# Performance work log

Hardware: AMD Instinct MI355X
Metric: run time of the kernel (lower is better)

## Reference

```python
import jax, jax.numpy as jnp
import numpy as np

B, N, C, H = 16, 577, 768, 12
D = C // H
BETA = 1.0
KEEP_RATIO = 0.5


def setup_inputs() -> dict:
    key = jax.random.key(0)
    k0, k1, k2, k3 = jax.random.split(key, 4)
    x = jax.random.normal(k0, (B, N, C), dtype=jnp.float32)
    # UCB visit-count buffer, strictly positive as accumulated counts would be
    ucb_count_score = jax.random.uniform(k1, (H, N), dtype=jnp.float32) * 50.0 + 1.0
    Wqkv = jax.random.normal(k2, (3 * C, C), dtype=jnp.float32) * 0.02
    Wproj = jax.random.normal(k3, (C, C), dtype=jnp.float32) * 0.02
    bproj = jnp.zeros((C,), dtype=jnp.float32)
    counter = 60  # > 50 so pruning path is taken
    return {"x": x, "ucb_count_score": ucb_count_score, "Wqkv": Wqkv,
            "Wproj": Wproj, "bproj": bproj, "counter": counter}


def reference(x, ucb_count_score, Wqkv, Wproj, bproj, counter):
    # UCBAttention.forward with pruning_enabled=True, selection_mode='ucb',
    # ucb_update_enabled=True, exclude_cls=True, dropout=0 (eval).
    Bs, Ns, Cs = x.shape
    scale = D ** -0.5
    k_keep = max(1, int((Ns - 1) * KEEP_RATIO))  # _get_k with keep_ratio

    qkv = (x @ Wqkv.T).reshape(Bs, Ns, 3, H, D).transpose(2, 0, 3, 1, 4)  # [3,B,H,N,D]
    q, k, v = qkv[0], qkv[1], qkv[2]
    attn_scores = jnp.einsum('bhqd,bhkd->bhqk', q, k) * scale
    attn_probs = jax.nn.softmax(attn_scores, axis=-1)  # [B,H,N,N]

    # UCB scores over patches (CLS excluded)
    patch_scores = attn_probs[:, :, :, 1:].mean(axis=2)            # [B,H,N-1]
    expl = BETA * jnp.sqrt(jnp.log(counter + 1.0) / (ucb_count_score[:, 1:] + 1e-6))
    ucb_scores = patch_scores + expl[None, :, :]                   # [B,H,N-1]
    global_ucb = ucb_scores.mean(axis=1)                           # [B,N-1]
    _, topk_rel = jax.lax.top_k(global_ucb, k_keep)                # [B,k]
    kept = topk_rel + 1                                            # token indices

    # keep-vector: CLS (0) always kept; mask[i,j] = kept[i] OR kept[j]
    kv_mask = (jnp.zeros((Bs, Ns), attn_probs.dtype)
               .at[jnp.arange(Bs)[:, None], kept].set(1.0)
               .at[:, 0].set(1.0))                                 # [B,N]
    mask = jnp.maximum(kv_mask[:, None, :, None], kv_mask[:, None, None, :])  # [B,1,N,N]

    pruned = attn_probs * mask
    pruned = pruned / (pruned.sum(axis=-1, keepdims=True) + 1e-8)
    context = jnp.einsum('bhqk,bhkd->bhqd', pruned, v)             # [B,H,N,D]

    out = context.transpose(0, 2, 1, 3).reshape(Bs, Ns, Cs) @ Wproj.T + bproj

    # score_delta: +1/B at each kept token column, broadcast over heads
    delta = jnp.zeros((Ns,), jnp.float32).at[kept.reshape(-1)].add(1.0 / Bs)
    score_delta = jnp.broadcast_to(delta[None, :], ucb_count_score.shape)
    return out, score_delta, kept
```

## Files before the change

### kernel.cpp

```cpp
#include <hip/hip_runtime.h>
#include <cstdio>
#include <cstdint>

#define B_    16
#define N_    577
#define C_    768
#define H_    12
#define D_    64
#define KKEEP 288
#define SCALE 0.125f
#define LOG2E 1.4426950408889634f
#define M_TOT (B_ * N_)
#define NKT   24
#define PLROW ((size_t)N_ * 64)

typedef __bf16 bf16x8_t __attribute__((ext_vector_type(8)));
typedef __bf16 bf16x4_t __attribute__((ext_vector_type(4)));
typedef float  f32x4_t  __attribute__((ext_vector_type(4)));
typedef unsigned int u32x4_t __attribute__((ext_vector_type(4)));
typedef unsigned int u32x2_t __attribute__((ext_vector_type(2)));

__device__ __forceinline__ f32x4_t mfma_bf16(bf16x8_t a, bf16x8_t b, f32x4_t c) {
    return __builtin_amdgcn_mfma_f32_16x16x32_bf16(a, b, c, 0, 0, 0);
}

__device__ __forceinline__ void gload16(const ushort* g, ushort* l) {
    __builtin_amdgcn_global_load_lds(
        (const __attribute__((address_space(1))) void*)g,
        (__attribute__((address_space(3))) void*)l, 16, 0, 0);
}
#define VMCNT(n) asm volatile("s_waitcnt vmcnt(" #n ")" ::: "memory")
#define LGKM0()  asm volatile("s_waitcnt lgkmcnt(0)" ::: "memory")
#define SB() __builtin_amdgcn_sched_barrier(0)

__device__ __forceinline__ int xcd_swz(int bid, int nwg) {
    int q = nwg >> 3, r = nwg & 7;
    int xcd = bid & 7, off = bid >> 3;
    int base = (xcd < r) ? xcd * (q + 1) : r * (q + 1) + (xcd - r) * q;
    return base + off;
}

__device__ __forceinline__ void splitf(float x, unsigned int &hi, unsigned int &lo) {
    unsigned int u = __float_as_uint(x);
    hi = u >> 16;
    float r = x - __uint_as_float(u & 0xffff0000u);
    lo = __float_as_uint(r) >> 16;
}
__device__ __forceinline__ unsigned int bf16rne(float x) {
    unsigned int u = __float_as_uint(x);
    return (u + 0x7fffu + ((u >> 16) & 1u)) >> 16;
}

__device__ __forceinline__ void pack_tile(const float* __restrict__ src,
                                          ushort* __restrict__ dH,
                                          ushort* __restrict__ dL,
                                          int nrows, int tile) {
    int kt = tile % NKT, mt = tile / NKT;
    int w = threadIdx.x;
    int row = w >> 1, h = w & 1;
    int m = mt * 128 + row;
    int sw = (row >> 1) & 3;
    float f[16];
    if (m < nrows) {
        const float* s = src + (size_t)m * C_ + kt * 32;
        int sa = (2 * h) ^ sw, sb = (2 * h + 1) ^ sw;
        *(float4*)&f[0]  = *(const float4*)(s + sa * 8);
        *(float4*)&f[4]  = *(const float4*)(s + sa * 8 + 4);
        *(float4*)&f[8]  = *(const float4*)(s + sb * 8);
        *(float4*)&f[12] = *(const float4*)(s + sb * 8 + 4);
    } else {
#pragma unroll
        for (int i = 0; i < 16; i++) f[i] = 0.f;
    }
    unsigned hi[16], lo[16];
#pragma unroll
    for (int i = 0; i < 16; i++) splitf(f[i], hi[i], lo[i]);
    u32x4_t h0 = {hi[0] | (hi[1] << 16), hi[2] | (hi[3] << 16),
                  hi[4] | (hi[5] << 16), hi[6] | (hi[7] << 16)};
    u32x4_t h1 = {hi[8] | (hi[9] << 16), hi[10] | (hi[11] << 16),
                  hi[12] | (hi[13] << 16), hi[14] | (hi[15] << 16)};
    u32x4_t l0 = {lo[0] | (lo[1] << 16), lo[2] | (lo[3] << 16),
                  lo[4] | (lo[5] << 16), lo[6] | (lo[7] << 16)};
    u32x4_t l1 = {lo[8] | (lo[9] << 16), lo[10] | (lo[11] << 16),
                  lo[12] | (lo[13] << 16), lo[14] | (lo[15] << 16)};
    size_t dbase = (size_t)tile * 4096 + row * 32;
    *(u32x4_t*)&dH[dbase + (2 * h) * 8]     = h0;
    *(u32x4_t*)&dH[dbase + (2 * h + 1) * 8] = h1;
    *(u32x4_t*)&dL[dbase + (2 * h) * 8]     = l0;
    *(u32x4_t*)&dL[dbase + (2 * h + 1) * 8] = l1;
}

__device__ __forceinline__ void pack_tile_rne(const float* __restrict__ src,
                                              ushort* __restrict__ dst,
                                              int nrows, int tile) {
    int kt = tile % NKT, mt = tile / NKT;
    int w = threadIdx.x;
    int row = w >> 1, h = w & 1;
    int m = mt * 128 + row;
    int sw = (row >> 1) & 3;
    float f[16];
    if (m < nrows) {
        const float* s = src + (size_t)m * C_ + kt * 32;
        int sa = (2 * h) ^ sw, sb = (2 * h + 1) ^ sw;
        *(float4*)&f[0]  = *(const float4*)(s + sa * 8);
        *(float4*)&f[4]  = *(const float4*)(s + sa * 8 + 4);
        *(float4*)&f[8]  = *(const float4*)(s + sb * 8);
        *(float4*)&f[12] = *(const float4*)(s + sb * 8 + 4);
    } else {
#pragma unroll
        for (int i = 0; i < 16; i++) f[i] = 0.f;
    }
    unsigned hi[16];
#pragma unroll
    for (int i = 0; i < 16; i++) hi[i] = bf16rne(f[i]);
    u32x4_t h0 = {hi[0] | (hi[1] << 16), hi[2] | (hi[3] << 16),
                  hi[4] | (hi[5] << 16), hi[6] | (hi[7] << 16)};
    u32x4_t h1 = {hi[8] | (hi[9] << 16), hi[10] | (hi[11] << 16),
                  hi[12] | (hi[13] << 16), hi[14] | (hi[15] << 16)};
    size_t dbase = (size_t)tile * 4096 + row * 32;
    *(u32x4_t*)&dst[dbase + (2 * h) * 8]     = h0;
    *(u32x4_t*)&dst[dbase + (2 * h + 1) * 8] = h1;
}

#define NXP 1752
#define NWP 432
#define NPJ 144
#define NZ  37

__global__ __launch_bounds__(256) void pack_all_kernel(const float* __restrict__ x,
                                                       const float* __restrict__ Wqkv,
                                                       const float* __restrict__ Wproj,
                                                       ushort* __restrict__ XplH,
                                                       ushort* __restrict__ XplL,
                                                       ushort* __restrict__ WplH,
                                                       ushort* __restrict__ WplL,
                                                       ushort* __restrict__ Wpjb,
                                                       float* __restrict__ kvmask) {
    int bid = blockIdx.x;
    if (bid < NXP) {
        pack_tile(x, XplH, XplL, M_TOT, bid);
    } else if (bid < NXP + NWP) {
        pack_tile(Wqkv, WplH, WplL, 3 * C_, bid - NXP);
    } else if (bid < NXP + NWP + NPJ) {
        pack_tile_rne(Wproj, Wpjb, C_, bid - NXP - NWP);
    } else {
        int i = (bid - NXP - NWP - NPJ) * 256 + threadIdx.x;
        if (i < B_ * N_) kvmask[i] = 0.f;
    }
}

__device__ __forceinline__ bf16x8_t fragT(const ushort* H, int row, int c, int ls) {
    int phys = ((c << 2) + ls) ^ (row & 7);
    return __builtin_bit_cast(bf16x8_t, *(const u32x4_t*)&H[(row << 6) + (phys << 3)]);
}

__global__ __launch_bounds__(256) void gemm_qkv_mfma(const ushort* __restrict__ XplH,
                                                     const ushort* __restrict__ XplL,
                                                     const ushort* __restrict__ WplH,
                                                     const ushort* __restrict__ WplL,
                                                     ushort* __restrict__ qhp,
                                                     ushort* __restrict__ qlp,
                                                     ushort* __restrict__ khp,
                                                     ushort* __restrict__ klp,
                                                     ushort* __restrict__ vtp) {
    __shared__ ushort SMEM[32768];
    ushort* Ah = SMEM;
    ushort* Al = SMEM + 8192;
    ushort* Bh = SMEM + 16384;
    ushort* Bl = SMEM + 24576;
    const int bid = xcd_swz(blockIdx.x, 18 * 73);
    const int bx = bid % 18, by = bid / 18;
    const int tid = threadIdx.x;
    const int lane = tid & 63, wave = tid >> 6;
    const int wr = wave >> 1, wc = wave & 1;
    const int lr = lane & 15, ls = lane >> 4;
    const int m0 = by * 128;
    const int o0 = wave * 1024, o1 = o0 + 512;
    const int la = lane * 8;
    const size_t abase = (size_t)by * NKT * 4096;
    const size_t bbase = (size_t)bx * NKT * 4096;
    f32x4_t acc[4][4] = {};

    if (bx < 12) {
        auto stage = [&](int buf, int kt) {
            const size_t ta = abase + (size_t)kt * 4096;
            const size_t tb = bbase + (size_t)kt * 4096;
            gload16(XplH + ta + o0 + la, &Ah[buf * 4096 + o0]);
            gload16(XplH + ta + o1 + la, &Ah[buf * 4096 + o1]);
            gload16(XplL + ta + o0 + la, &Al[buf * 4096 + o0]);
            gload16(XplL + ta + o1 + la, &Al[buf * 4096 + o1]);
            gload16(WplH + tb + o0 + la, &Bh[buf * 4096 + o0]);
            gload16(WplH + tb + o1 + la, &Bh[buf * 4096 + o1]);
            gload16(WplL + tb + o0 + la, &Bl[buf * 4096 + o0]);
            gload16(WplL + tb + o1 + la, &Bl[buf * 4096 + o1]);
        };
        stage(0, 0);
#pragma unroll 1
        for (int kt = 0; kt < NKT; ++kt) {
            const int cur = kt & 1;
            if (kt + 1 < NKT) {
                stage(cur ^ 1, kt + 1);
                VMCNT(8);
            } else {
                VMCNT(0);
            }
            SB();
            __builtin_amdgcn_s_barrier();
            SB();
            bf16x8_t fah[4], fal[4], fbh[4], fbl[4];
#pragma unroll
            for (int i = 0; i < 4; i++) {
                int rowA = wr * 64 + i * 16 + lr;
                int pa = ls ^ ((rowA >> 1) & 3);
                fah[i] = __builtin_bit_cast(bf16x8_t, *(const u32x4_t*)&Ah[cur * 4096 + rowA * 32 + pa * 8]);
                fal[i] = __builtin_bit_cast(bf16x8_t, *(const u32x4_t*)&Al[cur * 4096 + rowA * 32 + pa * 8]);
                int rowB = wc * 64 + i * 16 + lr;
                int pb = ls ^ ((rowB >> 1) & 3);
                fbh[i] = __builtin_bit_cast(bf16x8_t, *(const u32x4_t*)&Bh[cur * 4096 + rowB * 32 + pb * 8]);
                fbl[i] = __builtin_bit_cast(bf16x8_t, *(const u32x4_t*)&Bl[cur * 4096 + rowB * 32 + pb * 8]);
            }
#pragma unroll
            for (int i = 0; i < 4; i++)
#pragma unroll
                for (int j = 0; j < 4; j++) {
                    acc[i][j] = mfma_bf16(fah[i], fbh[j], acc[i][j]);
                    acc[i][j] = mfma_bf16(fah[i], fbl[j], acc[i][j]);
                    acc[i][j] = mfma_bf16(fal[i], fbh[j], acc[i][j]);
                }
            if (kt + 1 < NKT) {
                SB();
                __builtin_amdgcn_s_barrier();
            }
        }
        const int n0 = bx * 128;
        const int s = n0 / C_;
        __syncthreads();
        unsigned* T = (unsigned*)SMEM;
        const float sc = (s == 0) ? SCALE * LOG2E : 1.0f;
#pragma unroll
        for (int j = 0; j < 4; j++) {
            int nl = wc * 64 + j * 16 + lr;
#pragma unroll
            for (int i = 0; i < 4; i++) {
#pragma unroll
                for (int r = 0; r < 4; r++) {
                    int ml = wr * 64 + i * 16 + ls * 4 + r;
                    unsigned hi, lo;
                    splitf(acc[i][j][r] * sc, hi, lo);
                    int idx = ml * 128 + ((((nl >> 3) ^ ((ml >> 2) & 7)) << 3) | (nl & 7));
                    T[idx] = hi | (lo << 16);
                }
            }
        }
        __syncthreads();
        ushort* dh = (s == 1) ? khp : qhp;
        ushort* dl = (s == 1) ? klp : qlp;
        const int hh0 = (n0 % C_) / D_;
#pragma unroll
        for (int it = 0; it < 8; ++it) {
            int g = it * 256 + tid;
            int sl = g & 7;
            int m_local = (g >> 3) & 127;
            int hh_half = g >> 10;
            int m = m0 + m_local;
            if (m < M_TOT) {
                int b = m / N_, n = m % N_;
                int dg = sl ^ (n & 7);
                int grp = (hh_half * 8 + dg) ^ ((m_local >> 2) & 7);
                const unsigned* src = &T[m_local * 128 + grp * 8];
                u32x4_t a = *(const u32x4_t*)src;
                u32x4_t bvv = *(const u32x4_t*)(src + 4);
                u32x4_t hiv = {(a[0] & 0xffffu) | (a[1] << 16),
                               (a[2] & 0xffffu) | (a[3] << 16),
                               (bvv[0] & 0xffffu) | (bvv[1] << 16),
                               (bvv[2] & 0xffffu) | (bvv[3] << 16)};
                u32x4_t lov = {(a[0] >> 16) | (a[1] & 0xffff0000u),
                               (a[2] >> 16) | (a[3] & 0xffff0000u),
                               (bvv[0] >> 16) | (bvv[1] & 0xffff0000u),
                               (bvv[2] >> 16) | (bvv[3] & 0xffff0000u)};
                size_t off = (size_t)(b * H_ + hh0 + hh_half) * PLROW + (size_t)n * 64 + sl * 8;
                *(u32x4_t*)&dh[off] = hiv;
                *(u32x4_t*)&dl[off] = lov;
            }
        }
    } else {
        auto stage = [&](int buf, int kt) {
            const size_t ta = abase + (size_t)kt * 4096;
            const size_t tb = bbase + (size_t)kt * 4096;
            gload16(XplH + ta + o0 + la, &Ah[buf * 4096 + o0]);
            gload16(XplH + ta + o1 + la, &Ah[buf * 4096 + o1]);
            gload16(XplL + ta + o0 + la, &Al[buf * 4096 + o0]);
            gload16(XplL + ta + o1 + la, &Al[buf * 4096 + o1]);
            gload16(WplH + tb + o0 + la, &Bh[buf * 4096 + o0]);
            gload16(WplH + tb + o1 + la, &Bh[buf * 4096 + o1]);
        };
        stage(0, 0);
#pragma unroll 1
        for (int kt = 0; kt < NKT; ++kt) {
            const int cur = kt & 1;
            if (kt + 1 < NKT) {
                stage(cur ^ 1, kt + 1);
                VMCNT(6);
            } else {
                VMCNT(0);
            }
            SB();
            __builtin_amdgcn_s_barrier();
            SB();
            bf16x8_t fah[4], fal[4], fbh[4];
#pragma unroll
            for (int i = 0; i < 4; i++) {
                int rowA = wr * 64 + i * 16 + lr;
                int pa = ls ^ ((rowA >> 1) & 3);
                fah[i] = __builtin_bit_cast(bf16x8_t, *(const u32x4_t*)&Ah[cur * 4096 + rowA * 32 + pa * 8]);
                fal[i] = __builtin_bit_cast(bf16x8_t, *(const u32x4_t*)&Al[cur * 4096 + rowA * 32 + pa * 8]);
                int rowB = wc * 64 + i * 16 + lr;
                int pb = ls ^ ((rowB >> 1) & 3);
                fbh[i] = __builtin_bit_cast(bf16x8_t, *(const u32x4_t*)&Bh[cur * 4096 + rowB * 32 + pb * 8]);
            }
#pragma unroll
            for (int i = 0; i < 4; i++)
#pragma unroll
                for (int j = 0; j < 4; j++) {
                    acc[i][j] = mfma_bf16(fah[i], fbh[j], acc[i][j]);
                    acc[i][j] = mfma_bf16(fal[i], fbh[j], acc[i][j]);
                }
            if (kt + 1 < NKT) {
                SB();
                __builtin_amdgcn_s_barrier();
            }
        }
        const int n0v = (bx - 12) * 128;
#pragma unroll
        for (int j = 0; j < 4; j++) {
            int ng = n0v + wc * 64 + j * 16 + lr;
            int hh = ng / D_;
            int d = ng % D_;
#pragma unroll
            for (int i = 0; i < 4; i++) {
                int mg0 = m0 + wr * 64 + i * 16 + ls * 4;
#pragma unroll
                for (int r = 0; r < 4; r++) {
                    int m = mg0 + r;
                    if (m < M_TOT) {
                        int b = m / N_, n = m % N_;
                        int jt = n >> 6, jl = n & 63;
                        size_t off = ((size_t)(b * H_ + hh) * 10 + jt) * 4096 +
                                     (size_t)d * 64 + (((jl >> 3) ^ (d & 7)) << 3) + (jl & 7);
                        vtp[off] = __builtin_bit_cast(unsigned short, (__bf16)acc[i][j][r]);
                    }
                }
            }
        }
    }
}

__global__ __launch_bounds__(512) void attn_rowsum_mfma(const ushort* __restrict__ qh,
                                                        const ushort* __restrict__ ql,
                                                        const ushort* __restrict__ kh,
                                                        const ushort* __restrict__ kl,
                                                        float* __restrict__ w) {
    __shared__ ushort Qh[8192], Ql[8192];
    __shared__ ushort Kh[4096], Kl[4096];
    __shared__ float red[8][64];
    const int bid = xcd_swz(blockIdx.x, 5 * B_ * H_);
    const int bh = bid / 5, q0 = (bid % 5) * 128;
    const int tid = threadIdx.x, lane = tid & 63, wv = tid >> 6;
    const int wg = wv >> 2, wl = wv & 3;
    const int lr = lane & 15, ls = lane >> 4;
    const size_t bho = (size_t)bh * PLROW;
    const ushort* qhp = qh + bho; const ushort* qlp = ql + bho;
    const ushort* khp = kh + bho; const ushort* klp = kl + bho;
    auto qrow = [&](int rr) { return (size_t)min(q0 + wv * 16 + rr * 8 + (lane >> 3), N_ - 1) * 64 + (lane & 7) * 8; };
    gload16(qhp + qrow(0), &Qh[wv * 1024]);
    gload16(qhp + qrow(1), &Qh[wv * 1024 + 512]);
    gload16(qlp + qrow(0), &Ql[wv * 1024]);
    gload16(qlp + qrow(1), &Ql[wv * 1024 + 512]);
    auto krow = [&](int j0) { return (size_t)min(j0 + wv * 8 + (lane >> 3), N_ - 1) * 64 + (lane & 7) * 8; };
    auto stageK = [&](int j0) {
        gload16(khp + krow(j0), &Kh[wv * 512]);
        gload16(klp + krow(j0), &Kl[wv * 512]);
    };
    stageK(0);
    VMCNT(0);
    __syncthreads();
    bf16x8_t fqh[4][2], fql[4][2];
#pragma unroll
    for (int i = 0; i < 4; i++)
#pragma unroll
        for (int c = 0; c < 2; c++) {
            fqh[i][c] = fragT(Qh, wg * 64 + i * 16 + lr, c, ls);
            fql[i][c] = fragT(Ql, wg * 64 + i * 16 + lr, c, ls);
        }
    float rs[4] = {0.f, 0.f, 0.f, 0.f};
#pragma unroll 1
    for (int t = 0; t < 10; ++t) {
        bf16x8_t fkh[2], fkl[2];
#pragma unroll
        for (int c = 0; c < 2; c++) {
            fkh[c] = fragT(Kh, wl * 16 + lr, c, ls);
            fkl[c] = fragT(Kl, wl * 16 + lr, c, ls);
        }
        LGKM0(); SB();
        __builtin_amdgcn_s_barrier();
        SB();
        if (t < 9) stageK((t + 1) * 64);
        int jbase = t * 64 + wl * 16 + ls * 4;
#pragma unroll
        for (int i = 0; i < 4; i++) {
            f32x4_t s = {0.f, 0.f, 0.f, 0.f};
            __builtin_amdgcn_s_setprio(1);
#pragma unroll
            for (int c = 0; c < 2; c++) {
                s = mfma_bf16(fkh[c], fqh[i][c], s);
                s = mfma_bf16(fkh[c], fql[i][c], s);
                s = mfma_bf16(fkl[c], fqh[i][c], s);
            }
            __builtin_amdgcn_s_setprio(0);
#pragma unroll
            for (int r = 0; r < 4; r++)
                rs[i] += (jbase + r < N_) ? __builtin_amdgcn_exp2f(s[r]) : 0.f;
        }
        if (t < 9) {
            VMCNT(0); SB();
            __builtin_amdgcn_s_barrier();
            SB();
        }
    }
#pragma unroll
    for (int i = 0; i < 4; i++) {
        float v2 = rs[i];
        v2 += __shfl_xor(v2, 16);
        v2 += __shfl_xor(v2, 32);
        if (ls == 0) red[wv][i * 16 + lr] = v2;
    }
    __syncthreads();
    if (tid < 128) {
        int grp = tid >> 6, qlc = tid & 63;
        float s = red[grp * 4 + 0][qlc] + red[grp * 4 + 1][qlc] +
                  red[grp * 4 + 2][qlc] + red[grp * 4 + 3][qlc];
        int qn = q0 + tid;
        if (qn < N_) w[(size_t)bh * N_ + qn] = 1.0f / s;
    }
}

__global__ __launch_bounds__(512) void attn_colsum_mfma(const ushort* __restrict__ qh,
                                                        const ushort* __restrict__ ql,
                                                        const ushort* __restrict__ kh,
                                                        const ushort* __restrict__ kl,
                                                        const float* __restrict__ w,
                                                        float* __restrict__ colsum) {
    __shared__ ushort KhS[8192], KlS[8192];
    __shared__ ushort Qh[4096], Ql[4096];
    __shared__ float wsAll[640];
    __shared__ float red[8][64];
    const int bid = xcd_swz(blockIdx.x, 5 * B_ * H_);
    const int bh = bid / 5, j0 = (bid % 5) * 128;
    const int tid = threadIdx.x, lane = tid & 63, wv = tid >> 6;
    const int wg = wv >> 2, wl = wv & 3;
    const int lr = lane & 15, ls = lane >> 4;
    const size_t bho = (size_t)bh * PLROW;
    const ushort* qhp = qh + bho; const ushort* qlp = ql + bho;
    const ushort* khp = kh + bho; const ushort* klp = kl + bho;
    auto krow = [&](int rr) { return (size_t)min(j0 + wv * 16 + rr * 8 + (lane >> 3), N_ - 1) * 64 + (lane & 7) * 8; };
    gload16(khp + krow(0), &KhS[wv * 1024]);
    gload16(khp + krow(1), &KhS[wv * 1024 + 512]);
    gload16(klp + krow(0), &KlS[wv * 1024]);
    gload16(klp + krow(1), &KlS[wv * 1024 + 512]);
    auto qrow2 = [&](int qt) { return (size_t)min(qt + wv * 8 + (lane >> 3), N_ - 1) * 64 + (lane & 7) * 8; };
    auto stageQ = [&](int qt) {
        gload16(qhp + qrow2(qt), &Qh[wv * 512]);
        gload16(qlp + qrow2(qt), &Ql[wv * 512]);
    };
    stageQ(0);
    for (int i2 = tid; i2 < 640; i2 += 512)
        wsAll[i2] = (i2 < N_) ? w[(size_t)bh * N_ + i2] : 0.f;
    VMCNT(0);
    __syncthreads();
    bf16x8_t fkh[4][2], fkl[4][2];
#pragma unroll
    for (int i = 0; i < 4; i++)
#pragma unroll
        for (int c = 0; c < 2; c++) {
            fkh[i][c] = fragT(KhS, wg * 64 + i * 16 + lr, c, ls);
            fkl[i][c] = fragT(KlS, wg * 64 + i * 16 + lr, c, ls);
        }
    float cs[4] = {0.f, 0.f, 0.f, 0.f};
#pragma unroll 1
    for (int t = 0; t < 10; ++t) {
        bf16x8_t fqh[2], fql[2];
#pragma unroll
        for (int c = 0; c < 2; c++) {
            fqh[c] = fragT(Qh, wl * 16 + lr, c, ls);
            fql[c] = fragT(Ql, wl * 16 + lr, c, ls);
        }
        float wq[4];
#pragma unroll
        for (int r = 0; r < 4; r++) wq[r] = wsAll[t * 64 + wl * 16 + ls * 4 + r];
        LGKM0(); SB();
        __builtin_amdgcn_s_barrier();
        SB();
        if (t < 9) stageQ((t + 1) * 64);
#pragma unroll
        for (int i = 0; i < 4; i++) {
            f32x4_t s = {0.f, 0.f, 0.f, 0.f};
            __builtin_amdgcn_s_setprio(1);
#pragma unroll
            for (int c = 0; c < 2; c++) {
                s = mfma_bf16(fqh[c], fkh[i][c], s);
                s = mfma_bf16(fql[c], fkh[i][c], s);
                s = mfma_bf16(fqh[c], fkl[i][c], s);
            }
            __builtin_amdgcn_s_setprio(0);
#pragma unroll
            for (int r = 0; r < 4; r++) cs[i] += __builtin_amdgcn_exp2f(s[r]) * wq[r];
        }
        if (t < 9) {
            VMCNT(0); SB();
            __builtin_amdgcn_s_barrier();
            SB();
        }
    }
#pragma unroll
    for (int i = 0; i < 4; i++) {
        float v2 = cs[i];
        v2 += __shfl_xor(v2, 16);
        v2 += __shfl_xor(v2, 32);
        if (ls == 0) red[wv][i * 16 + lr] = v2;
    }
    __syncthreads();
    if (tid < 128) {
        int grp = tid >> 6, jlc = tid & 63;
        float t2 = red[grp * 4 + 0][jlc] + red[grp * 4 + 1][jlc] +
                   red[grp * 4 + 2][jlc] + red[grp * 4 + 3][jlc];
        int jn = j0 + tid;
        if (jn < N_) colsum[(size_t)bh * N_ + jn] = t2;
    }
}

__global__ __launch_bounds__(512) void topk_kernel(const float* __restrict__ colsum,
                                                   const float* __restrict__ ucb_count,
                                                   const int* __restrict__ counter,
                                                   float* __restrict__ kept_out,
                                                   float* __restrict__ kvmask) {
    __shared__ float sv[1024];
    __shared__ int si[1024];
    int b = blockIdx.x, tid = threadIdx.x;
    float lc = logf((float)counter[0] + 1.0f);
    for (int t = tid; t < 1024; t += 512) {
        if (t < N_ - 1) {
            int tok = t + 1;
            float accv = 0.f;
#pragma unroll
            for (int h = 0; h < H_; h++) {
                float csv = colsum[(size_t)(b * H_ + h) * N_ + tok];
                float patch = csv * (1.0f / (float)N_);
                float cnt = ucb_count[h * N_ + tok];
                float expl = sqrtf(lc / (cnt + 1e-6f));
                accv += patch + expl;
            }
            sv[t] = accv * (1.0f / (float)H_);
            si[t] = t;
        } else {
            sv[t] = -INFINITY;
            si[t] = 1 << 20;
        }
    }
    __syncthreads();
    for (int kk = 2; kk <= 1024; kk <<= 1) {
        for (int jj = kk >> 1; jj > 0; jj >>= 1) {
            for (int t = tid; t < 1024; t += 512) {
                int ixj = t ^ jj;
                if (ixj > t) {
                    float v1 = sv[t], v2 = sv[ixj];
                    int i1 = si[t], i2 = si[ixj];
                    bool before21 = (v2 > v1) || (v2 == v1 && i2 < i1);
                    bool dirDesc = ((t & kk) == 0);
                    if (before21 == dirDesc) {
                        sv[t] = v2; sv[ixj] = v1;
                        si[t] = i2; si[ixj] = i1;
                    }
                }
            }
            __syncthreads();
        }
    }
    for (int r = tid; r < KKEEP; r += 512) {
        int tok = si[r] + 1;
        kept_out[b * KKEEP + r] = (float)tok;
        kvmask[b * N_ + tok] = 1.0f;
    }
    if (tid == 0) kvmask[b * N_] = 1.0f;
}

__global__ __launch_bounds__(512) void attn_ctx_mfma(const ushort* __restrict__ qh,
                                                     const ushort* __restrict__ ql,
                                                     const ushort* __restrict__ kh,
                                                     const ushort* __restrict__ vtp,
                                                     const float* __restrict__ kvmask,
                                                     ushort* __restrict__ ctxb,
                                                     float* __restrict__ sd) {
    if (blockIdx.x >= 5 * B_ * H_) {
        int idx = (blockIdx.x - 5 * B_ * H_) * 512 + threadIdx.x;
        if (idx < H_ * N_) {
            int n = idx % N_;
            float d = 0.f;
            if (n != 0) {
#pragma unroll
                for (int b = 0; b < B_; b++) d += kvmask[b * N_ + n];
            }
            sd[idx] = d * (1.0f / (float)B_);
        }
        return;
    }
    __shared__ ushort Kh[4096], Vt[4096];
    __shared__ ushort Pl[2][4096];
    __shared__ float mkAll[640];
    float (*red)[64] = (float(*)[64])&Pl[0][0];
    float* inv = (float*)&Pl[1][0];
    const int bid = xcd_swz(blockIdx.x, 5 * B_ * H_);
    const int bh = bid / 5, q0 = (bid % 5) * 128;
    const int b = bh / H_, h = bh % H_;
    const int tid = threadIdx.x, lane = tid & 63, wv = tid >> 6;
    const int wg = wv >> 2, wl = wv & 3;
    const int lr = lane & 15, ls = lane >> 4;
    const size_t bho = (size_t)bh * PLROW;
    const ushort* qhp = qh + bho; const ushort* qlp = ql + bho;
    const ushort* khp = kh + bho;
    const ushort* vtb = vtp + (size_t)bh * 10 * 4096;
    ushort* PlS = &Pl[0][0];
    for (int i2 = tid; i2 < 640; i2 += 512)
        mkAll[i2] = (i2 < N_) ? kvmask[(size_t)b * N_ + i2] : 0.f;
    auto qrow = [&](int rr) { return (size_t)min(q0 + wv * 16 + rr * 8 + (lane >> 3), N_ - 1) * 64 + (lane & 7) * 8; };
    bf16x8_t fqh[4][2], fql[4][2];
    gload16(qhp + qrow(0), &PlS[wv * 1024]);
    gload16(qhp + qrow(1), &PlS[wv * 1024 + 512]);
    VMCNT(0); __syncthreads();
#pragma unroll
    for (int i = 0; i < 4; i++)
#pragma unroll
        for (int c = 0; c < 2; c++)
            fqh[i][c] = fragT(PlS, wg * 64 + i * 16 + lr, c, ls);
    __syncthreads();
    gload16(qlp + qrow(0), &PlS[wv * 1024]);
    gload16(qlp + qrow(1), &PlS[wv * 1024 + 512]);
    VMCNT(0); __syncthreads();
#pragma unroll
    for (int i = 0; i < 4; i++)
#pragma unroll
        for (int c = 0; c < 2; c++)
            fql[i][c] = fragT(PlS, wg * 64 + i * 16 + lr, c, ls);
    __syncthreads();
    auto krow = [&](int j0) { return (size_t)min(j0 + wv * 8 + (lane >> 3), N_ - 1) * 64 + (lane & 7) * 8; };
    auto stageKV = [&](int t) {
        gload16(khp + krow(t * 64), &Kh[wv * 512]);
        gload16(vtb + (size_t)t * 4096 + wv * 512 + lane * 8, &Vt[wv * 512]);
    };
    float mq[4];
#pragma unroll
    for (int i = 0; i < 4; i++) mq[i] = mkAll[q0 + wg * 64 + i * 16 + lr];
    stageKV(0);
    VMCNT(0);
    SB(); __builtin_amdgcn_s_barrier(); SB();
    f32x4_t acc[4] = {};
    float psums[4] = {0.f, 0.f, 0.f, 0.f};
#pragma unroll 1
    for (int t = 0; t < 10; ++t) {
        bf16x8_t fkh[2], fv[2];
#pragma unroll
        for (int c = 0; c < 2; c++) {
            fkh[c] = fragT(Kh, wl * 16 + lr, c, ls);
            fv[c]  = fragT(Vt, wl * 16 + lr, c, ls);
        }
        LGKM0(); SB();
        __builtin_amdgcn_s_barrier();
        SB();
        if (t < 9) stageKV(t + 1);
        int jloc = wl * 16 + ls * 4;
        float jmv[4], jbias[4];
#pragma unroll
        for (int r = 0; r < 4; r++) {
            int j = t * 64 + jloc + r;
            jmv[r] = mkAll[t * 64 + jloc + r];
            jbias[r] = (j < N_) ? 0.f : -16384.f;
        }
#pragma unroll
        for (int i = 0; i < 4; i++) {
            f32x4_t s = {0.f, 0.f, 0.f, 0.f};
            __builtin_amdgcn_s_setprio(1);
#pragma unroll
            for (int c = 0; c < 2; c++) {
                s = mfma_bf16(fkh[c], fqh[i][c], s);
                s = mfma_bf16(fkh[c], fql[i][c], s);
            }
            __builtin_amdgcn_s_setprio(0);
            bf16x4_t pb;
            float mqi = mq[i];
#pragma unroll
            for (int r = 0; r < 4; r++) {
                float p = __builtin_amdgcn_exp2f(s[r] + jbias[r]) * fmaxf(mqi, jmv[r]);
                psums[i] += p;
                pb[r] = (__bf16)p;
            }
            int row = i * 16 + lr;
            int slot = ((wl << 1) + (ls >> 1)) ^ (row & 7);
            *(u32x2_t*)&Pl[wg][(row << 6) + (slot << 3) + ((ls & 1) << 2)] =
                __builtin_bit_cast(u32x2_t, pb);
        }
        SB(); LGKM0(); SB();
        __builtin_amdgcn_s_barrier();
        SB();
        __builtin_amdgcn_s_setprio(1);
#pragma unroll
        for (int i = 0; i < 4; i++) {
            bf16x8_t fp0 = fragT(Pl[wg], i * 16 + lr, 0, ls);
            bf16x8_t fp1 = fragT(Pl[wg], i * 16 + lr, 1, ls);
            acc[i] = mfma_bf16(fv[0], fp0, acc[i]);
            acc[i] = mfma_bf16(fv[1], fp1, acc[i]);
        }
        __builtin_amdgcn_s_setprio(0);
        if (t < 9) {
            VMCNT(0); SB();
            __builtin_amdgcn_s_barrier();
            SB();
        }
    }
    __syncthreads();
#pragma unroll
    for (int i = 0; i < 4; i++) {
        float v2 = psums[i];
        v2 += __shfl_xor(v2, 16);
        v2 += __shfl_xor(v2, 32);
        if (ls == 0) red[wv][i * 16 + lr] = v2;
    }
    __syncthreads();
    if (tid < 128) {
        int grp = tid >> 6, qlc = tid & 63;
        float t2 = red[grp * 4 + 0][qlc] + red[grp * 4 + 1][qlc] +
                   red[grp * 4 + 2][qlc] + red[grp * 4 + 3][qlc];
        inv[tid] = 1.0f / (t2 + 1e-8f);
    }
    __syncthreads();
#pragma unroll
    for (int i = 0; i < 4; i++) {
        int qn = q0 + wg * 64 + i * 16 + lr;
        if (qn < N_) {
            float rn = inv[wg * 64 + i * 16 + lr];
            bf16x4_t ov;
            ov[0] = (__bf16)(acc[i][0] * rn);
            ov[1] = (__bf16)(acc[i][1] * rn);
            ov[2] = (__bf16)(acc[i][2] * rn);
            ov[3] = (__bf16)(acc[i][3] * rn);
            int m = b * N_ + qn;
            int col = h * D_ + wl * 16 + ls * 4;
            int mt = m >> 7, rowl = m & 127;
            int kt2 = col >> 5, c32 = col & 31;
            int phys = (c32 >> 3) ^ ((rowl >> 1) & 3);
            size_t off = ((size_t)(mt * NKT + kt2)) * 4096 + rowl * 32 + phys * 8 + (c32 & 7);
            *(u32x2_t*)&ctxb[off] = __builtin_bit_cast(u32x2_t, ov);
        }
    }
}

__global__ __launch_bounds__(256) void gemm_proj_mfma(const ushort* __restrict__ Apl,
                                                      const ushort* __restrict__ Bpl,
                                                      const float* __restrict__ bias,
                                                      float* __restrict__ out) {
    __shared__ ushort Ab[2][4096], Bb[2][4096];
    const int bid = xcd_swz(blockIdx.x, 6 * 73);
    const int bx = bid % 6, by = bid / 6;
    const int tid = threadIdx.x;
    const int lane = tid & 63, wave = tid >> 6;
    const int wr = wave >> 1, wc = wave & 1;
    const int lr = lane & 15, ls = lane >> 4;
    const int m0 = by * 128, n0 = bx * 128;
    const int o0 = wave * 1024, o1 = o0 + 512;
    const int la = lane * 8;
    const size_t abase = (size_t)by * NKT * 4096;
    const size_t bbase = (size_t)bx * NKT * 4096;
    f32x4_t acc[4][4] = {};

    auto stage = [&](int buf, int kt) {
        const size_t ta = abase + (size_t)kt * 4096;
        const size_t tb = bbase + (size_t)kt * 4096;
        gload16(Apl + ta + o0 + la, &Ab[buf][o0]);
        gload16(Apl + ta + o1 + la, &Ab[buf][o1]);
        gload16(Bpl + tb + o0 + la, &Bb[buf][o0]);
        gload16(Bpl + tb + o1 + la, &Bb[buf][o1]);
    };
    stage(0, 0);
#pragma unroll 1
    for (int kt = 0; kt < NKT; ++kt) {
        const int cur = kt & 1;
        if (kt + 1 < NKT) {
            stage(cur ^ 1, kt + 1);
            VMCNT(4);
        } else {
            VMCNT(0);
        }
        SB();
        __builtin_amdgcn_s_barrier();
        SB();
        bf16x8_t fa[4], fb[4];
#pragma unroll
        for (int i = 0; i < 4; i++) {
            int rowA = wr * 64 + i * 16 + lr;
            int pa = ls ^ ((rowA >> 1) & 3);
            fa[i] = __builtin_bit_cast(bf16x8_t, *(const u32x4_t*)&Ab[cur][rowA * 32 + pa * 8]);
            int rowB = wc * 64 + i * 16 + lr;
            int pb = ls ^ ((rowB >> 1) & 3);
            fb[i] = __builtin_bit_cast(bf16x8_t, *(const u32x4_t*)&Bb[cur][rowB * 32 + pb * 8]);
        }
#pragma unroll
        for (int i = 0; i < 4; i++)
#pragma unroll
            for (int j = 0; j < 4; j++)
                acc[i][j] = mfma_bf16(fa[i], fb[j], acc[i][j]);
        if (kt + 1 < NKT) {
            SB();
            __builtin_amdgcn_s_barrier();
        }
    }
#pragma unroll
    for (int j = 0; j < 4; j++) {
        int ng = n0 + wc * 64 + j * 16 + lr;
        float bb = bias[ng];
#pragma unroll
        for (int i = 0; i < 4; i++) {
            int mg0 = m0 + wr * 64 + i * 16 + ls * 4;
#pragma unroll
            for (int r = 0; r < 4; r++) {
                int m = mg0 + r;
                if (m < M_TOT) out[(size_t)m * C_ + ng] = acc[i][j][r] + bb;
            }
        }
    }
}

extern "C" void kernel_launch(void* const* d_in, const int* in_sizes, int n_in,
                              void* d_out, int out_size, void* d_ws, size_t ws_size,
                              hipStream_t stream) {
    const float* x     = (const float*)d_in[0];
    const float* ucb   = (const float*)d_in[1];
    const float* Wqkv  = (const float*)d_in[2];
    const float* Wproj = (const float*)d_in[3];
    const float* bproj = (const float*)d_in[4];
    const int*   counter = (const int*)d_in[5];

    const size_t BHN  = (size_t)B_ * H_ * N_;
    const size_t XPL  = (size_t)(73 * 128) * C_;
    const size_t WPL  = (size_t)3 * C_ * C_;
    const size_t WPJ  = (size_t)C_ * C_;
    const size_t PLN  = (size_t)192 * PLROW;
    const size_t VTSZ = (size_t)192 * 10 * 4096;

    ushort* qhp  = (ushort*)d_ws;
    ushort* qlp  = qhp + PLN;
    ushort* khp  = qlp + PLN;
    ushort* klp  = khp + PLN;
    ushort* vtp  = klp + PLN;
    ushort* XplH = vtp + VTSZ;
    ushort* XplL = XplH + XPL;
    ushort* ctxb = XplH;
    ushort* WplH = XplL + XPL;
    ushort* WplL = WplH + WPL;
    ushort* Wpjb = WplL + WPL;
    float*  w    = (float*)(Wpjb + WPJ);
    float*  colsum = w + BHN;
    float*  kvmask = colsum + BHN;
    size_t need = ((char*)(kvmask + (size_t)B_ * N_)) - (char*)d_ws;
    if (ws_size < need) {
        fprintf(stderr, "kernel_launch: ws too small, need %zu have %zu\n",
                need, ws_size);
        return;
    }

    float* out  = (float*)d_out;
    float* sd   = out + (size_t)B_ * N_ * C_;
    float* kept = sd + (size_t)H_ * N_;

    pack_all_kernel<<<NXP + NWP + NPJ + NZ, 256, 0, stream>>>(
        x, Wqkv, Wproj, XplH, XplL, WplH, WplL, Wpjb, kvmask);

    gemm_qkv_mfma<<<18 * 73, 256, 0, stream>>>(XplH, XplL, WplH, WplL,
                                               qhp, qlp, khp, klp, vtp);
    attn_rowsum_mfma<<<5 * B_ * H_, 512, 0, stream>>>(qhp, qlp, khp, klp, w);
    attn_colsum_mfma<<<5 * B_ * H_, 512, 0, stream>>>(qhp, qlp, khp, klp, w, colsum);
    topk_kernel<<<B_, 512, 0, stream>>>(colsum, ucb, counter, kept, kvmask);
    attn_ctx_mfma<<<5 * B_ * H_ + 14, 512, 0, stream>>>(qhp, qlp, khp, vtp,
                                                        kvmask, ctxb, sd);
    gemm_proj_mfma<<<6 * 73, 256, 0, stream>>>(ctxb, Wpjb, bproj, out);
}
```

Baseline: 275.0 us.

## Shrink QKV GEMM LDS by single-buffering B tiles and splitting epilogue

The QKV projection GEMM now double-buffers only the activation (A) tiles and keeps the weight (B) tiles in a single buffer. The next B tile is loaded after the fragments are read and a barrier, overlapping with the MFMA block, which runs at raised wave priority. The Q/K epilogue transpose is done in two 64-row rounds so it fits in the smaller LDS, cutting shared memory from 64KB to 48KB per block to allow more resident blocks. In exchange each k-step gets an extra barrier and a full vmcnt wait, so B-tile load latency is less hidden.

```diff
diff --git a/kernel.cpp b/kernel.cpp
--- a/kernel.cpp
+++ b/kernel.cpp
@@ -163,11 +163,11 @@
                                                      ushort* __restrict__ khp,
                                                      ushort* __restrict__ klp,
                                                      ushort* __restrict__ vtp) {
-    __shared__ ushort SMEM[32768];
+    __shared__ ushort SMEM[24576];
     ushort* Ah = SMEM;
     ushort* Al = SMEM + 8192;
     ushort* Bh = SMEM + 16384;
-    ushort* Bl = SMEM + 24576;
+    ushort* Bl = SMEM + 20480;
     const int bid = xcd_swz(blockIdx.x, 18 * 73);
     const int bx = bid % 18, by = bid / 18;
     const int tid = threadIdx.x;
@@ -182,31 +182,28 @@
     f32x4_t acc[4][4] = {};
 
     if (bx < 12) {
-        auto stage = [&](int buf, int kt) {
+        auto stageA = [&](int buf, int kt) {
             const size_t ta = abase + (size_t)kt * 4096;
-            const size_t tb = bbase + (size_t)kt * 4096;
             gload16(XplH + ta + o0 + la, &Ah[buf * 4096 + o0]);
             gload16(XplH + ta + o1 + la, &Ah[buf * 4096 + o1]);
             gload16(XplL + ta + o0 + la, &Al[buf * 4096 + o0]);
             gload16(XplL + ta + o1 + la, &Al[buf * 4096 + o1]);
-            gload16(WplH + tb + o0 + la, &Bh[buf * 4096 + o0]);
-            gload16(WplH + tb + o1 + la, &Bh[buf * 4096 + o1]);
-            gload16(WplL + tb + o0 + la, &Bl[buf * 4096 + o0]);
-            gload16(WplL + tb + o1 + la, &Bl[buf * 4096 + o1]);
         };
-        stage(0, 0);
+        auto stageB = [&](int kt) {
+            const size_t tb = bbase + (size_t)kt * 4096;
+            gload16(WplH + tb + o0 + la, &Bh[o0]);
+            gload16(WplH + tb + o1 + la, &Bh[o1]);
+            gload16(WplL + tb + o0 + la, &Bl[o0]);
+            gload16(WplL + tb + o1 + la, &Bl[o1]);
+        };
+        stageA(0, 0);
+        stageB(0);
+        VMCNT(0);
+        SB(); __builtin_amdgcn_s_barrier(); SB();
 #pragma unroll 1
         for (int kt = 0; kt < NKT; ++kt) {
             const int cur = kt & 1;
-            if (kt + 1 < NKT) {
-                stage(cur ^ 1, kt + 1);
-                VMCNT(8);
-            } else {
-                VMCNT(0);
-            }
-            SB();
-            __builtin_amdgcn_s_barrier();
-            SB();
+            if (kt + 1 < NKT) stageA(cur ^ 1, kt + 1);
             bf16x8_t fah[4], fal[4], fbh[4], fbl[4];
 #pragma unroll
             for (int i = 0; i < 4; i++) {
@@ -216,9 +213,14 @@
                 fal[i] = __builtin_bit_cast(bf16x8_t, *(const u32x4_t*)&Al[cur * 4096 + rowA * 32 + pa * 8]);
                 int rowB = wc * 64 + i * 16 + lr;
                 int pb = ls ^ ((rowB >> 1) & 3);
-                fbh[i] = __builtin_bit_cast(bf16x8_t, *(const u32x4_t*)&Bh[cur * 4096 + rowB * 32 + pb * 8]);
-                fbl[i] = __builtin_bit_cast(bf16x8_t, *(const u32x4_t*)&Bl[cur * 4096 + rowB * 32 + pb * 8]);
-            }
+                fbh[i] = __builtin_bit_cast(bf16x8_t, *(const u32x4_t*)&Bh[rowB * 32 + pb * 8]);
+                fbl[i] = __builtin_bit_cast(bf16x8_t, *(const u32x4_t*)&Bl[rowB * 32 + pb * 8]);
+            }
+            LGKM0(); SB();
+            __builtin_amdgcn_s_barrier();
+            SB();
+            if (kt + 1 < NKT) stageB(kt + 1);
+            __builtin_amdgcn_s_setprio(1);
 #pragma unroll
             for (int i = 0; i < 4; i++)
 #pragma unroll
@@ -227,9 +229,11 @@
                     acc[i][j] = mfma_bf16(fah[i], fbl[j], acc[i][j]);
                     acc[i][j] = mfma_bf16(fal[i], fbh[j], acc[i][j]);
                 }
+            __builtin_amdgcn_s_setprio(0);
             if (kt + 1 < NKT) {
+                VMCNT(0); SB();
+                __builtin_amdgcn_s_barrier();
                 SB();
-                __builtin_amdgcn_s_barrier();
             }
         }
         const int n0 = bx * 128;
@@ -237,76 +241,81 @@
         __syncthreads();
         unsigned* T = (unsigned*)SMEM;
         const float sc = (s == 0) ? SCALE * LOG2E : 1.0f;
-#pragma unroll
-        for (int j = 0; j < 4; j++) {
-            int nl = wc * 64 + j * 16 + lr;
-#pragma unroll
-            for (int i = 0; i < 4; i++) {
-#pragma unroll
-                for (int r = 0; r < 4; r++) {
-                    int ml = wr * 64 + i * 16 + ls * 4 + r;
-                    unsigned hi, lo;
-                    splitf(acc[i][j][r] * sc, hi, lo);
-                    int idx = ml * 128 + ((((nl >> 3) ^ ((ml >> 2) & 7)) << 3) | (nl & 7));
-                    T[idx] = hi | (lo << 16);
-                }
-            }
-        }
-        __syncthreads();
         ushort* dh = (s == 1) ? khp : qhp;
         ushort* dl = (s == 1) ? klp : qlp;
         const int hh0 = (n0 % C_) / D_;
-#pragma unroll
-        for (int it = 0; it < 8; ++it) {
-            int g = it * 256 + tid;
-            int sl = g & 7;
-            int m_local = (g >> 3) & 127;
-            int hh_half = g >> 10;
-            int m = m0 + m_local;
-            if (m < M_TOT) {
-                int b = m / N_, n = m % N_;
-                int dg = sl ^ (n & 7);
-                int grp = (hh_half * 8 + dg) ^ ((m_local >> 2) & 7);
-                const unsigned* src = &T[m_local * 128 + grp * 8];
-                u32x4_t a = *(const u32x4_t*)src;
-                u32x4_t bvv = *(const u32x4_t*)(src + 4);
-                u32x4_t hiv = {(a[0] & 0xffffu) | (a[1] << 16),
-                               (a[2] & 0xffffu) | (a[3] << 16),
-                               (bvv[0] & 0xffffu) | (bvv[1] << 16),
-                               (bvv[2] & 0xffffu) | (bvv[3] << 16)};
-                u32x4_t lov = {(a[0] >> 16) | (a[1] & 0xffff0000u),
-                               (a[2] >> 16) | (a[3] & 0xffff0000u),
-                               (bvv[0] >> 16) | (bvv[1] & 0xffff0000u),
-                               (bvv[2] >> 16) | (bvv[3] & 0xffff0000u)};
-                size_t off = (size_t)(b * H_ + hh0 + hh_half) * PLROW + (size_t)n * 64 + sl * 8;
-                *(u32x4_t*)&dh[off] = hiv;
-                *(u32x4_t*)&dl[off] = lov;
-            }
+#pragma unroll 1
+        for (int round = 0; round < 2; ++round) {
+            if (wr == round) {
+#pragma unroll
+                for (int j = 0; j < 4; j++) {
+                    int nl = wc * 64 + j * 16 + lr;
+#pragma unroll
+                    for (int i = 0; i < 4; i++) {
+#pragma unroll
+                        for (int r = 0; r < 4; r++) {
+                            int ml = wr * 64 + i * 16 + ls * 4 + r;
+                            unsigned hi, lo;
+                            splitf(acc[i][j][r] * sc, hi, lo);
+                            int idx = (ml & 63) * 128 +
+                                      ((((nl >> 3) ^ ((ml >> 2) & 7)) << 3) | (nl & 7));
+                            T[idx] = hi | (lo << 16);
+                        }
+                    }
+                }
+            }
+            __syncthreads();
+#pragma unroll
+            for (int it = 0; it < 4; ++it) {
+                int g = it * 256 + tid;
+                int sl = g & 7;
+                int m_local64 = (g >> 3) & 63;
+                int hh_half = g >> 9;
+                int m_local = round * 64 + m_local64;
+                int m = m0 + m_local;
+                if (m < M_TOT) {
+                    int b = m / N_, n = m % N_;
+                    int dg = sl ^ (n & 7);
+                    int grp = (hh_half * 8 + dg) ^ ((m_local >> 2) & 7);
+                    const unsigned* src = &T[m_local64 * 128 + grp * 8];
+                    u32x4_t a = *(const u32x4_t*)src;
+                    u32x4_t bvv = *(const u32x4_t*)(src + 4);
+                    u32x4_t hiv = {(a[0] & 0xffffu) | (a[1] << 16),
+                                   (a[2] & 0xffffu) | (a[3] << 16),
+                                   (bvv[0] & 0xffffu) | (bvv[1] << 16),
+                                   (bvv[2] & 0xffffu) | (bvv[3] << 16)};
+                    u32x4_t lov = {(a[0] >> 16) | (a[1] & 0xffff0000u),
+                                   (a[2] >> 16) | (a[3] & 0xffff0000u),
+                                   (bvv[0] >> 16) | (bvv[1] & 0xffff0000u),
+                                   (bvv[2] >> 16) | (bvv[3] & 0xffff0000u)};
+                    size_t off = (size_t)(b * H_ + hh0 + hh_half) * PLROW + (size_t)n * 64 + sl * 8;
+                    *(u32x4_t*)&dh[off] = hiv;
+                    *(u32x4_t*)&dl[off] = lov;
+                }
+            }
+            if (round == 0) __syncthreads();
         }
     } else {
-        auto stage = [&](int buf, int kt) {
+        auto stageA = [&](int buf, int kt) {
             const size_t ta = abase + (size_t)kt * 4096;
-            const size_t tb = bbase + (size_t)kt * 4096;
             gload16(XplH + ta + o0 + la, &Ah[buf * 4096 + o0]);
             gload16(XplH + ta + o1 + la, &Ah[buf * 4096 + o1]);
             gload16(XplL + ta + o0 + la, &Al[buf * 4096 + o0]);
             gload16(XplL + ta + o1 + la, &Al[buf * 4096 + o1]);
-            gload16(WplH + tb + o0 + la, &Bh[buf * 4096 + o0]);
-            gload16(WplH + tb + o1 + la, &Bh[buf * 4096 + o1]);
         };
-        stage(0, 0);
+        auto stageB = [&](int kt) {
+            const size_t tb = bbase + (size_t)kt * 4096;
+            gload16(WplH + tb + o0 + la, &Bh[o0]);
+            gload16(WplH + tb + o1 + la, &Bh[o1]);
+        };
+        stageA(0, 0);
+        stageB(0);
+        VMCNT(0);
+        SB(); __builtin_amdgcn_s_barrier(); SB();
 #pragma unroll 1
         for (int kt = 0; kt < NKT; ++kt) {
             const int cur = kt & 1;
-            if (kt + 1 < NKT) {
-                stage(cur ^ 1, kt + 1);
-                VMCNT(6);
-            } else {
-                VMCNT(0);
-            }
-            SB();
-            __builtin_amdgcn_s_barrier();
-            SB();
+            if (kt + 1 < NKT) stageA(cur ^ 1, kt + 1);
             bf16x8_t fah[4], fal[4], fbh[4];
 #pragma unroll
             for (int i = 0; i < 4; i++) {
@@ -316,8 +325,13 @@
                 fal[i] = __builtin_bit_cast(bf16x8_t, *(const u32x4_t*)&Al[cur * 4096 + rowA * 32 + pa * 8]);
                 int rowB = wc * 64 + i * 16 + lr;
                 int pb = ls ^ ((rowB >> 1) & 3);
-                fbh[i] = __builtin_bit_cast(bf16x8_t, *(const u32x4_t*)&Bh[cur * 4096 + rowB * 32 + pb * 8]);
-            }
+                fbh[i] = __builtin_bit_cast(bf16x8_t, *(const u32x4_t*)&Bh[rowB * 32 + pb * 8]);
+            }
+            LGKM0(); SB();
+            __builtin_amdgcn_s_barrier();
+            SB();
+            if (kt + 1 < NKT) stageB(kt + 1);
+            __builtin_amdgcn_s_setprio(1);
 #pragma unroll
             for (int i = 0; i < 4; i++)
 #pragma unroll
@@ -325,9 +339,11 @@
                     acc[i][j] = mfma_bf16(fah[i], fbh[j], acc[i][j]);
                     acc[i][j] = mfma_bf16(fal[i], fbh[j], acc[i][j]);
                 }
+            __builtin_amdgcn_s_setprio(0);
             if (kt + 1 < NKT) {
+                VMCNT(0); SB();
+                __builtin_amdgcn_s_barrier();
                 SB();
-                __builtin_amdgcn_s_barrier();
             }
         }
         const int n0v = (bx - 12) * 128;
```

Result: no change. 271.1 us, median of 2 (-1.4%).
